# Kernel tuning notes

Hardware: AMD Instinct MI355X
Metric: run time of the kernel (lower is better)

The kernel has to match this reference:

```python
import jax, jax.numpy as jnp
import numpy as np

NEG_SLOPE = 0.2  # PyG GATConv default negative_slope
N_GRAPHS = 128


def gat_conv(x, src, dst, w, a_src, a_dst, b):
    """PyG GATConv (v1), concat=True. x:[N,F], src/dst:[E] (self-loops included),
    w:[F,H*C], a_src/a_dst:[H,C], b:[H*C]."""
    N = x.shape[0]
    H, C = a_src.shape
    h = (x @ w).reshape(N, H, C)                      # [N,H,C]
    e = (h * a_src).sum(-1)[src] + (h * a_dst).sum(-1)[dst]  # [E,H]
    e = jnp.where(e > 0, e, NEG_SLOPE * e)            # leaky_relu
    m = jax.ops.segment_max(e, dst, num_segments=N)   # per-dst softmax max
    ex = jnp.exp(e - m[dst])
    s = jax.ops.segment_sum(ex, dst, num_segments=N)
    alpha = ex / (s[dst] + 1e-16)                     # [E,H]
    out = jax.ops.segment_sum(h[src] * alpha[:, :, None], dst, num_segments=N)
    return out.reshape(N, H * C) + b


def pool(x, batch, num_graphs):
    """concat(global_mean_pool, global_max_pool)."""
    ones = jnp.ones((x.shape[0],), x.dtype)
    cnt = jax.ops.segment_sum(ones, batch, num_segments=num_graphs)
    mean = jax.ops.segment_sum(x, batch, num_segments=num_graphs) / jnp.maximum(cnt, 1.0)[:, None]
    mx = jax.ops.segment_max(x, batch, num_segments=num_graphs)
    return jnp.concatenate([mean, mx], axis=-1)


def setup_inputs() -> dict:
    key = jax.random.key(0)
    ks = jax.random.split(key, 30)
    N, E, G = 100000, 800000, N_GRAPHS
    F_in, H, C = 260, 4, 64
    HC = H * C  # 256

    def lin(k, i, o):
        return (jax.random.normal(k, (i, o), jnp.float32) * (1.0 / np.sqrt(i)))

    def att(k):
        return jax.random.normal(k, (H, C), jnp.float32) * 0.1

    return {
        "x": jax.random.normal(ks[0], (N, F_in), jnp.float32),
        "edge_index": jax.random.randint(ks[1], (2, E), 0, N),
        "batch": jnp.sort(jax.random.randint(ks[2], (N,), 0, G)),
        "gat1_w": lin(ks[3], F_in, HC), "gat1_as": att(ks[4]), "gat1_ad": att(ks[5]),
        "gat1_b": jnp.zeros((HC,), jnp.float32),
        "lin1_w": lin(ks[6], HC, C), "lin1_b": jnp.zeros((C,), jnp.float32),
        "gat2_w": lin(ks[7], C, HC), "gat2_as": att(ks[8]), "gat2_ad": att(ks[9]),
        "gat2_b": jnp.zeros((HC,), jnp.float32),
        "lin2_w": lin(ks[10], HC, C), "lin2_b": jnp.zeros((C,), jnp.float32),
        "sum_w": lin(ks[11], 4 * C, 2 * C), "sum_b": jnp.zeros((2 * C,), jnp.float32),
        "sh1_w": lin(ks[12], 2 * C, C), "sh1_b": jnp.zeros((C,), jnp.float32),
        "sh2_w": lin(ks[13], C, C), "sh2_b": jnp.zeros((C,), jnp.float32),
        "sh3_w": lin(ks[14], C, C), "sh3_b": jnp.zeros((C,), jnp.float32),
        "reg_w": lin(ks[15], C, 32), "reg_b": jnp.zeros((32,), jnp.float32),
    }


def reference(x, edge_index, batch,
              gat1_w, gat1_as, gat1_ad, gat1_b, lin1_w, lin1_b,
              gat2_w, gat2_as, gat2_ad, gat2_b, lin2_w, lin2_b,
              sum_w, sum_b, sh1_w, sh1_b, sh2_w, sh2_b, sh3_w, sh3_b,
              reg_w, reg_b):
    N = x.shape[0]
    loop = jnp.arange(N)
    src = jnp.concatenate([edge_index[0], loop])  # add_self_loops=True
    dst = jnp.concatenate([edge_index[1], loop])

    h = gat_conv(x, src, dst, gat1_w, gat1_as, gat1_ad, gat1_b)
    h = jax.nn.selu(h @ lin1_w + lin1_b)
    x1 = pool(h, batch, N_GRAPHS)                 # [G, 2C]

    h = gat_conv(h, src, dst, gat2_w, gat2_as, gat2_ad, gat2_b)
    h = jax.nn.selu(h @ lin2_w + lin2_b)
    x2 = pool(h, batch, N_GRAPHS)                 # [G, 2C]

    z = jnp.concatenate([x1, x2], axis=-1) @ sum_w + sum_b
    z = jax.nn.selu(z @ sh1_w + sh1_b)
    z = jax.nn.selu(z @ sh2_w + sh2_b)
    z = jax.nn.selu(z @ sh3_w + sh3_b)
    return z @ reg_w + reg_b                      # [G, 32]
```

## Files before the change

kernel.cpp:

```cpp
#include <hip/hip_runtime.h>
#include <hip/hip_bf16.h>
#include <cstdint>

#define NEG_SLOPE 0.2f
#define HEADS 4
#define CH 64
#define HC 256
#define F_IN 260
#define KPAD1 288
#define NGRAPH 128

typedef __attribute__((ext_vector_type(8))) short bf16x8;
typedef __attribute__((ext_vector_type(8))) unsigned short u16x8;
typedef __attribute__((ext_vector_type(4))) float f32x4;

__device__ __forceinline__ float seluf(float x){
    const float sc=1.0507009873554805f, al=1.6732632423543772f;
    return x>0.f ? sc*x : sc*al*(__expf(x)-1.f);
}
__device__ __forceinline__ unsigned fenc(float x){
    unsigned u=__float_as_uint(x);
    return (u&0x80000000u)? ~u : (u|0x80000000u);
}
__device__ __forceinline__ float fdec(unsigned e){
    unsigned u = (e&0x80000000u)? (e&0x7fffffffu) : ~e;
    return __uint_as_float(u);
}
__device__ __forceinline__ float bf2f(unsigned short u){
    return __uint_as_float(((unsigned)u)<<16);
}
__device__ __forceinline__ unsigned short f2bf_raw(float x){
    unsigned u = __float_as_uint(x);
    unsigned rounded = u + 0x7fffu + ((u >> 16) & 1u);
    return (unsigned short)(rounded >> 16);
}
__device__ __forceinline__ void gload_lds16(const void* g, void* l){
    __builtin_amdgcn_global_load_lds(
        (const __attribute__((address_space(1))) void*)g,
        (__attribute__((address_space(3))) void*)l, 16, 0, 0);
}

__global__ void fill_u32_kernel(unsigned* p, unsigned v, int n){
    int i = blockIdx.x*blockDim.x + threadIdx.x;
    for (; i<n; i += gridDim.x*blockDim.x) p[i]=v;
}

__global__ void degree_kernel(const int* __restrict__ ei, int* __restrict__ deg, int E){
    int i = blockIdx.x*blockDim.x+threadIdx.x;
    for (; i<E; i+=gridDim.x*blockDim.x) atomicAdd(&deg[ei[E+i]], 1);
}

__global__ void scan_ph1(const int* __restrict__ deg, int* __restrict__ bsum, int N){
    __shared__ int sd[256];
    int base = blockIdx.x*1024;
    int t = threadIdx.x;
    int tot=0;
    for(int u=0;u<4;u++){ int i = base + t*4+u; tot += (i<N)? deg[i]:0; }
    sd[t]=tot; __syncthreads();
    for(int off=128; off; off>>=1){ if(t<off) sd[t]+=sd[t+off]; __syncthreads(); }
    if(t==0) bsum[blockIdx.x]=sd[0];
}
__global__ void scan_ph2(int* bsum, int nb, int* rowptr, int N, int E){
    if(threadIdx.x==0 && blockIdx.x==0){
        int run=0;
        for(int b=0;b<nb;b++){ int v=bsum[b]; bsum[b]=run; run+=v; }
        rowptr[N]=E;
    }
}
__global__ void scan_ph3(const int* __restrict__ deg, const int* __restrict__ bsum,
                         int* __restrict__ rowptr, int N){
    __shared__ int sd[256];
    int base = blockIdx.x*1024;
    int t = threadIdx.x;
    int v[4]; int tot=0;
    for(int u=0;u<4;u++){ int i=base+t*4+u; v[u] = (i<N)? deg[i]:0; tot+=v[u]; }
    sd[t]=tot; __syncthreads();
    for(int off=1; off<256; off<<=1){
        int add = (t>=off)? sd[t-off] : 0;
        __syncthreads();
        sd[t] += add;
        __syncthreads();
    }
    int pre = bsum[blockIdx.x] + ((t==0)?0: sd[t-1]);
    for(int u=0;u<4;u++){ int i=base+t*4+u; if(i<N){ rowptr[i]=pre; pre+=v[u]; } }
}

__global__ void scatter_kernel(const int* __restrict__ ei, const int* __restrict__ rowptr,
                               int* __restrict__ fil, int* __restrict__ col, int E){
    int i = blockIdx.x*blockDim.x+threadIdx.x;
    for(; i<E; i+=gridDim.x*blockDim.x){
        int s = ei[i], d = ei[E+i];
        int p = atomicAdd(&fil[d],1);
        col[rowptr[d]+p] = s;
    }
}

__global__ void cvt_x_kernel(const float* __restrict__ x, unsigned* __restrict__ xb, int N){
    int i = blockIdx.x*blockDim.x+threadIdx.x;
    int total = N*36;
    for (; i<total; i+=gridDim.x*blockDim.x){
        int row = i/36;
        int c = (i - row*36)*8;
        const float* src = x + (size_t)row*F_IN + c;
        float v[8];
        if (c + 8 <= F_IN){
            float4 a = *(const float4*)src;
            float4 b = *(const float4*)(src+4);
            v[0]=a.x; v[1]=a.y; v[2]=a.z; v[3]=a.w;
            v[4]=b.x; v[5]=b.y; v[6]=b.z; v[7]=b.w;
        } else {
            #pragma unroll
            for (int k=0;k<8;k++) v[k] = (c+k < F_IN) ? src[k] : 0.f;
        }
        unsigned d[4];
        #pragma unroll
        for (int k=0;k<4;k++)
            d[k] = (unsigned)f2bf_raw(v[2*k]) | ((unsigned)f2bf_raw(v[2*k+1])<<16);
        *(int4*)(xb + (size_t)row*144 + (c>>1)) = make_int4((int)d[0],(int)d[1],(int)d[2],(int)d[3]);
    }
}

__global__ void cvt_wT_kernel(const float* __restrict__ w, __hip_bfloat16* __restrict__ wt,
                              int K, int NC, int Kpad){
    int i = blockIdx.x*blockDim.x+threadIdx.x;
    if (i >= NC*Kpad) return;
    int n = i / Kpad, k = i - n*Kpad;
    wt[i] = __float2bfloat16(k < K ? w[(size_t)k*NC + n] : 0.f);
}

template<int BN, int FS, int POOL, int STORE>
__global__ __launch_bounds__(512, 4) void mfma_gemm_kernel(
    const __hip_bfloat16* __restrict__ A, int Kpad,
    const __hip_bfloat16* __restrict__ Bt,
    const float* __restrict__ bias, int act,
    __hip_bfloat16* __restrict__ Cb,
    const float* __restrict__ asrc, const float* __restrict__ adst,
    float* __restrict__ ss, float* __restrict__ sdv,
    const int* __restrict__ batch, float* __restrict__ psum,
    unsigned* __restrict__ pmax, int* __restrict__ cnt,
    int M, int NC)
{
    constexpr int NF = BN/32;
    constexpr int WN = BN/2;
    constexpr int TP = WN + 8;
    constexpr int STAGE = 16384 + 2*BN*64;
    constexpr int LDSB  = POOL ? (STAGE + 128*72*2) : 32768;
    __shared__ __align__(16) char lds[LDSB];

    int tid  = threadIdx.x;
    int lane = tid & 63;
    int w    = tid >> 6;
    int wr = w >> 1, wc = w & 1;
    int row0 = blockIdx.x * 128;
    int col0 = blockIdx.y * BN;
    int fr   = lane & 15;
    int koff = (lane >> 4) * 16;

    f32x4 acc[2][NF];
    #pragma unroll
    for (int i=0;i<2;i++)
        #pragma unroll
        for (int j=0;j<NF;j++) acc[i][j] = (f32x4){0.f,0.f,0.f,0.f};

    int lrow = lane >> 2;
    int lcolB = (lane & 3) * 16;
    int ktiles = Kpad >> 5;

    auto stage = [&](int kt, int pb){
        int k0b = kt*64;
        char* Asb = lds + pb*8192;
        char* Bsb = lds + 16384 + pb*(BN*64);
        {
            int gr = row0 + w*16 + lrow; if (gr > M-1) gr = M-1;
            gload_lds16((const char*)A + (size_t)gr*Kpad*2 + k0b + lcolB,
                        Asb + w*1024 + lrow*64 + lcolB);
        }
        if (w < BN/16){
            int gn = col0 + w*16 + lrow;
            gload_lds16((const char*)Bt + (size_t)gn*Kpad*2 + k0b + lcolB,
                        Bsb + w*1024 + lrow*64 + lcolB);
        }
    };

    stage(0, 0);
    __syncthreads();
    for (int kt=0; kt<ktiles; kt++){
        int pb = kt & 1;
        if (kt+1 < ktiles) stage(kt+1, pb^1);
        const char* Ab = lds + pb*8192;
        const char* Bb = lds + 16384 + pb*(BN*64);
        bf16x8 a[2], b[NF];
        a[0] = *(const bf16x8*)(Ab + (wr*32 +      fr)*64 + koff);
        a[1] = *(const bf16x8*)(Ab + (wr*32 + 16 + fr)*64 + koff);
        #pragma unroll
        for (int nt=0; nt<NF; nt++)
            b[nt] = *(const bf16x8*)(Bb + (wc*WN + nt*16 + fr)*64 + koff);
        #pragma unroll
        for (int mt=0; mt<2; mt++)
            #pragma unroll
            for (int nt=0; nt<NF; nt++)
                acc[mt][nt] = __builtin_amdgcn_mfma_f32_16x16x32_bf16(a[mt], b[nt], acc[mt][nt], 0, 0, 0);
        __syncthreads();
    }

    if (POOL){
        unsigned short* tile = (unsigned short*)(lds + STAGE);
        #pragma unroll
        for (int mt=0; mt<2; mt++)
            #pragma unroll
            for (int nt=0; nt<NF; nt++)
                #pragma unroll
                for (int r=0; r<4; r++){
                    float v = acc[mt][nt][r] + bias[wc*WN + nt*16 + fr];
                    v = seluf(v);
                    int tr = wr*32 + mt*16 + (lane>>4)*4 + r;
                    tile[tr*72 + wc*WN + nt*16 + fr] = f2bf_raw(v);
                }
        __syncthreads();
        if (STORE){
            #pragma unroll
            for (int p=0; p<2; p++){
                int idx = tid + p*512;
                int r = idx >> 3, ch = idx & 7;
                int gr = row0 + r;
                if (gr < M)
                    *(int4*)((char*)Cb + ((size_t)gr*NC + ch*8)*2) =
                        *(const int4*)((const char*)tile + r*144 + ch*16);
            }
        }
        int c  = tid & 63;
        int g8 = tid >> 6;
        float sum = 0.f, mx = -__builtin_inff();
        int cur = -1, rl = 0;
        #pragma unroll 1
        for (int j=0; j<16; j++){
            int r = g8*16 + j;
            int n = row0 + r;
            if (n >= M) break;
            int g = batch[n];
            if (g != cur){
                if (cur >= 0){
                    atomicAdd(&psum[cur*64+c], sum);
                    atomicMax(&pmax[cur*64+c], fenc(mx));
                    if (POOL==1 && c==0) atomicAdd(&cnt[cur], rl);
                }
                cur = g; sum = 0.f; mx = -__builtin_inff(); rl = 0;
            }
            float v = bf2f(tile[r*72 + c]);
            sum += v; mx = fmaxf(mx, v); rl++;
        }
        if (cur >= 0){
            atomicAdd(&psum[cur*64+c], sum);
            atomicMax(&pmax[cur*64+c], fenc(mx));
            if (POOL==1 && c==0) atomicAdd(&cnt[cur], rl);
        }
        return;
    }

    if (FS){
        float asv[NF], adv[NF];
        #pragma unroll
        for (int nt=0; nt<NF; nt++){
            int gc = col0 + wc*WN + nt*16 + fr;
            asv[nt] = asrc[gc];
            adv[nt] = adst[gc];
        }
        int head = (col0 + wc*WN) >> 6;
        #pragma unroll
        for (int mt=0; mt<2; mt++){
            #pragma unroll
            for (int r=0; r<4; r++){
                float ts=0.f, td=0.f;
                #pragma unroll
                for (int nt=0; nt<NF; nt++){
                    ts = fmaf(acc[mt][nt][r], asv[nt], ts);
                    td = fmaf(acc[mt][nt][r], adv[nt], td);
                }
                #pragma unroll
                for (int off=1; off<16; off<<=1){
                    ts += __shfl_xor(ts, off);
                    td += __shfl_xor(td, off);
                }
                if (fr==0){
                    int gr = row0 + wr*32 + mt*16 + (lane>>4)*4 + r;
                    if (gr < M){ ss[gr*4+head]=ts; sdv[gr*4+head]=td; }
                }
            }
        }
    }

    char* ct = lds + w*(16*TP*2);
    int c0 = col0 + wc*WN;
    #pragma unroll
    for (int mt=0; mt<2; mt++){
        #pragma unroll
        for (int nt=0; nt<NF; nt++){
            #pragma unroll
            for (int r=0; r<4; r++){
                float v = acc[mt][nt][r];
                if (bias) v += bias[c0 + nt*16 + fr];
                if (act)  v = seluf(v);
                int tr = (lane>>4)*4 + r;
                *(unsigned short*)(ct + tr*(TP*2) + (nt*16+fr)*2) = f2bf_raw(v);
            }
        }
        constexpr int CPR = WN/8;
        constexpr int RPP = 64/CPR;
        #pragma unroll
        for (int p=0; p<16/RPP; p++){
            int tr = p*RPP + lane/CPR;
            int ch = lane % CPR;
            int4 v = *(const int4*)(ct + tr*(TP*2) + ch*16);
            int gr = row0 + wr*32 + mt*16 + tr;
            if (gr < M)
                *(int4*)((char*)Cb + ((size_t)gr*NC + c0 + ch*8)*2) = v;
        }
    }
}

__global__ void aggregate_fused_kernel(const __hip_bfloat16* __restrict__ h,
                                       const float* __restrict__ ss, const float* __restrict__ sdv,
                                       const int* __restrict__ rowptr, const int* __restrict__ col,
                                       const float* __restrict__ bias,
                                       __hip_bfloat16* __restrict__ outp, int N){
    int node = blockIdx.x*4 + (threadIdx.x>>6);
    if (node >= N) return;
    int lane = threadIdx.x & 63;
    int s = lane >> 4;
    int t = lane & 15;
    int hh = t >> 2;
    const unsigned short* hp = (const unsigned short*)h;

    float ad = sdv[node*4+hh];
    float e0 = ss[node*4+hh] + ad;
    e0 = fmaxf(e0, NEG_SLOPE*e0);

    int jb = rowptr[node], je = rowptr[node+1];

    float m = (s==0) ? e0 : -1e30f;
    for (int j0 = jb; j0 < je; j0 += 8){
        int jA = j0 + s, jB = j0 + s + 4;
        if (jA < je){
            float e = ss[col[jA]*4+hh] + ad;
            m = fmaxf(m, fmaxf(e, NEG_SLOPE*e));
        }
        if (jB < je){
            float e = ss[col[jB]*4+hh] + ad;
            m = fmaxf(m, fmaxf(e, NEG_SLOPE*e));
        }
    }
    m = fmaxf(m, __shfl_xor(m, 16));
    m = fmaxf(m, __shfl_xor(m, 32));

    float acc[16];
    float psum;
    {
        float sa = (s==0) ? __expf(e0-m) : 0.f;
        psum = sa;
        const unsigned short* base = hp + (size_t)node*HC + t*16;
        u16x8 v0 = *(const u16x8*)(base);
        u16x8 v1 = *(const u16x8*)(base + 8);
        #pragma unroll
        for (int k=0;k<8;k++){
            acc[k]   = sa * bf2f(v0[k]);
            acc[8+k] = sa * bf2f(v1[k]);
        }
    }
    for (int j0 = jb; j0 < je; j0 += 8){
        int jA = j0 + s;
        int jB = j0 + s + 4;
        int scA = (jA < je) ? col[jA] : node;
        int scB = (jB < je) ? col[jB] : node;
        const unsigned short* bA = hp + (size_t)scA*HC + t*16;
        const unsigned short* bB = hp + (size_t)scB*HC + t*16;
        u16x8 a0 = *(const u16x8*)bA;
        u16x8 a1 = *(const u16x8*)(bA + 8);
        u16x8 b0 = *(const u16x8*)bB;
        u16x8 b1 = *(const u16x8*)(bB + 8);
        float eA = ss[scA*4+hh] + ad;
        float eB = ss[scB*4+hh] + ad;
        eA = fmaxf(eA, NEG_SLOPE*eA);
        eB = fmaxf(eB, NEG_SLOPE*eB);
        float pA = (jA < je) ? __expf(eA - m) : 0.f;
        float pB = (jB < je) ? __expf(eB - m) : 0.f;
        psum += pA + pB;
        #pragma unroll
        for (int k=0;k<8;k++){
            acc[k]   = fmaf(pA, bf2f(a0[k]), acc[k]);
            acc[8+k] = fmaf(pA, bf2f(a1[k]), acc[8+k]);
        }
        #pragma unroll
        for (int k=0;k<8;k++){
            acc[k]   = fmaf(pB, bf2f(b0[k]), acc[k]);
            acc[8+k] = fmaf(pB, bf2f(b1[k]), acc[8+k]);
        }
    }

    #pragma unroll
    for (int k=0;k<16;k++){
        acc[k] += __shfl_xor(acc[k], 16);
        acc[k] += __shfl_xor(acc[k], 32);
    }
    psum += __shfl_xor(psum, 16);
    psum += __shfl_xor(psum, 32);

    if (s==0){
        float inv = 1.f / psum;
        unsigned d[8];
        #pragma unroll
        for (int k=0;k<8;k++){
            unsigned lo = f2bf_raw(fmaf(acc[2*k],   inv, bias[t*16 + 2*k]));
            unsigned hi = f2bf_raw(fmaf(acc[2*k+1], inv, bias[t*16 + 2*k+1]));
            d[k] = lo | (hi<<16);
        }
        unsigned short* op = (unsigned short*)outp + (size_t)node*HC + t*16;
        int4 w0 = make_int4((int)d[0], (int)d[1], (int)d[2], (int)d[3]);
        int4 w1 = make_int4((int)d[4], (int)d[5], (int)d[6], (int)d[7]);
        *(int4*)op = w0;
        *(int4*)(op + 8) = w1;
    }
}

__global__ void pool_final_kernel(const float* __restrict__ psum, const unsigned* __restrict__ pmax,
                                  const int* __restrict__ cnt, float* __restrict__ x, int G){
    int i = blockIdx.x*blockDim.x+threadIdx.x;
    if (i >= G*64) return;
    int g=i>>6, c=i&63;
    float cf = fmaxf((float)cnt[g], 1.f);
    x[g*128 + c] = psum[i]/cf;
    x[g*128 + 64 + c] = fdec(pmax[i]);
}

__global__ __launch_bounds__(128) void head_kernel(
    const float* __restrict__ x1, const float* __restrict__ x2,
    const float* __restrict__ sw, const float* __restrict__ sb,
    const float* __restrict__ w1, const float* __restrict__ b1,
    const float* __restrict__ w2, const float* __restrict__ b2,
    const float* __restrict__ w3, const float* __restrict__ b3,
    const float* __restrict__ rw, const float* __restrict__ rb,
    float* __restrict__ out)
{
    int g = blockIdx.x, t = threadIdx.x;
    __shared__ float v[256], z1[128], z2[64], z3[64], z4[64];
    v[t] = x1[g*128+t];
    v[128+t] = x2[g*128+t];
    __syncthreads();
    float a = sb[t];
    for(int k=0;k<256;k++) a = fmaf(v[k], sw[k*128+t], a);
    z1[t] = a;
    __syncthreads();
    if(t<64){
        float a2 = b1[t];
        for(int k=0;k<128;k++) a2 = fmaf(z1[k], w1[k*64+t], a2);
        z2[t] = seluf(a2);
    }
    __syncthreads();
    if(t<64){
        float a3 = b2[t];
        for(int k=0;k<64;k++) a3 = fmaf(z2[k], w2[k*64+t], a3);
        z3[t] = seluf(a3);
    }
    __syncthreads();
    if(t<64){
        float a4 = b3[t];
        for(int k=0;k<64;k++) a4 = fmaf(z3[k], w3[k*64+t], a4);
        z4[t] = seluf(a4);
    }
    __syncthreads();
    if(t<32){
        float a5 = rb[t];
        for(int k=0;k<64;k++) a5 = fmaf(z4[k], rw[k*32+t], a5);
        out[g*32+t] = a5;
    }
}

extern "C" void kernel_launch(void* const* d_in, const int* in_sizes, int n_in,
                              void* d_out, int out_size, void* d_ws, size_t ws_size,
                              hipStream_t stream)
{
    const float* x    = (const float*)d_in[0];
    const int*   ei   = (const int*)d_in[1];
    const int*   batch= (const int*)d_in[2];
    const float* g1w  = (const float*)d_in[3];
    const float* g1as = (const float*)d_in[4];
    const float* g1ad = (const float*)d_in[5];
    const float* g1b  = (const float*)d_in[6];
    const float* l1w  = (const float*)d_in[7];
    const float* l1b  = (const float*)d_in[8];
    const float* g2w  = (const float*)d_in[9];
    const float* g2as = (const float*)d_in[10];
    const float* g2ad = (const float*)d_in[11];
    const float* g2b  = (const float*)d_in[12];
    const float* l2w  = (const float*)d_in[13];
    const float* l2b  = (const float*)d_in[14];
    const float* sw   = (const float*)d_in[15];
    const float* sb   = (const float*)d_in[16];
    const float* s1w  = (const float*)d_in[17];
    const float* s1b  = (const float*)d_in[18];
    const float* s2w  = (const float*)d_in[19];
    const float* s2b  = (const float*)d_in[20];
    const float* s3w  = (const float*)d_in[21];
    const float* s3b  = (const float*)d_in[22];
    const float* rw   = (const float*)d_in[23];
    const float* rb   = (const float*)d_in[24];
    float* out = (float*)d_out;

    const int N = in_sizes[0] / F_IN;
    const int E = in_sizes[1] / 2;
    const int G = NGRAPH;

    char* ws = (char*)d_ws;
    size_t off = 0;
    auto alloc = [&](size_t bytes)->void*{
        void* p = ws + off;
        off += (bytes + 255) & ~(size_t)255;
        return p;
    };
    int* deg     = (int*)alloc((size_t)2*N*4);
    int* fil     = deg + N;
    int* rowptr  = (int*)alloc(((size_t)N+1)*4);
    int* col     = (int*)alloc((size_t)E*4);
    int* bsum    = (int*)alloc(1024);
    int* zpool   = (int*)alloc((size_t)(128 + 2*G*64)*4);
    int*   cnt = zpool;
    float* PS1 = (float*)(zpool + 128);
    float* PS2 = PS1 + G*64;
    unsigned* PM1 = (unsigned*)alloc((size_t)2*G*64*4);
    unsigned* PM2 = PM1 + G*64;
    float* X1    = (float*)alloc((size_t)G*128*4);
    float* X2    = (float*)alloc((size_t)G*128*4);
    __hip_bfloat16* Xb  = (__hip_bfloat16*)alloc((size_t)N*KPAD1*2);
    __hip_bfloat16* W1t = (__hip_bfloat16*)alloc((size_t)HC*KPAD1*2);
    __hip_bfloat16* L1t = (__hip_bfloat16*)alloc((size_t)CH*HC*2);
    __hip_bfloat16* W2t = (__hip_bfloat16*)alloc((size_t)HC*CH*2);
    __hip_bfloat16* L2t = (__hip_bfloat16*)alloc((size_t)CH*HC*2);
    __hip_bfloat16* Abf = (__hip_bfloat16*)alloc((size_t)N*HC*2);
    __hip_bfloat16* Bbf = (__hip_bfloat16*)alloc((size_t)N*HC*2);
    __hip_bfloat16* HSb = (__hip_bfloat16*)alloc((size_t)N*CH*2);
    float* SCS   = (float*)alloc((size_t)N*HEADS*4);
    float* SCD   = (float*)alloc((size_t)N*HEADS*4);
    (void)ws_size; (void)n_in; (void)out_size;

    const unsigned ENC_NEG_INF = 0x007FFFFFu;
    int nb = (N+1023)/1024;

    fill_u32_kernel<<<256,256,0,stream>>>((unsigned*)deg, 0u, 2*N);
    fill_u32_kernel<<<64,256,0,stream>>>((unsigned*)zpool, 0u, 128 + 2*G*64);
    fill_u32_kernel<<<64,256,0,stream>>>(PM1, ENC_NEG_INF, 2*G*64);

    degree_kernel<<<1024,256,0,stream>>>(ei, deg, E);
    scan_ph1<<<nb,256,0,stream>>>(deg, bsum, N);
    scan_ph2<<<1,64,0,stream>>>(bsum, nb, rowptr, N, E);
    scan_ph3<<<nb,256,0,stream>>>(deg, bsum, rowptr, N);
    scatter_kernel<<<1024,256,0,stream>>>(ei, rowptr, fil, col, E);

    cvt_x_kernel<<<2048,256,0,stream>>>(x, (unsigned*)Xb, N);
    cvt_wT_kernel<<<(HC*KPAD1+255)/256,256,0,stream>>>(g1w, W1t, F_IN, HC, KPAD1);
    cvt_wT_kernel<<<(CH*HC+255)/256,256,0,stream>>>(l1w, L1t, HC, CH, HC);
    cvt_wT_kernel<<<(HC*CH+255)/256,256,0,stream>>>(g2w, W2t, CH, HC, CH);
    cvt_wT_kernel<<<(CH*HC+255)/256,256,0,stream>>>(l2w, L2t, HC, CH, HC);

    int nodeBlocks = (N+3)/4;
    dim3 gA((N+127)/128, 2);
    dim3 gL((N+127)/128, 1);

    mfma_gemm_kernel<128,1,0,1><<<gA,512,0,stream>>>(Xb, KPAD1, W1t, nullptr, 0, Abf,
                                                     g1as, g1ad, SCS, SCD,
                                                     nullptr, nullptr, nullptr, nullptr, N, HC);
    aggregate_fused_kernel<<<nodeBlocks,256,0,stream>>>(Abf, SCS, SCD, rowptr, col, g1b, Bbf, N);
    mfma_gemm_kernel<64,0,1,1><<<gL,512,0,stream>>>(Bbf, HC, L1t, l1b, 1, HSb,
                                                    nullptr, nullptr, nullptr, nullptr,
                                                    batch, PS1, PM1, cnt, N, CH);
    pool_final_kernel<<<(G*64+255)/256,256,0,stream>>>(PS1, PM1, cnt, X1, G);

    mfma_gemm_kernel<128,1,0,1><<<gA,512,0,stream>>>(HSb, CH, W2t, nullptr, 0, Abf,
                                                     g2as, g2ad, SCS, SCD,
                                                     nullptr, nullptr, nullptr, nullptr, N, HC);
    aggregate_fused_kernel<<<nodeBlocks,256,0,stream>>>(Abf, SCS, SCD, rowptr, col, g2b, Bbf, N);
    mfma_gemm_kernel<64,0,2,0><<<gL,512,0,stream>>>(Bbf, HC, L2t, l2b, 1, nullptr,
                                                    nullptr, nullptr, nullptr, nullptr,
                                                    batch, PS2, PM2, nullptr, N, CH);
    pool_final_kernel<<<(G*64+255)/256,256,0,stream>>>(PS2, PM2, cnt, X2, G);

    head_kernel<<<G,128,0,stream>>>(X1, X2, sw, sb, s1w, s1b, s2w, s2b, s3w, s3b, rw, rb, out);
}
```

Before: 462.7 us.

## Fuse fp32-to-bf16 input conversion into first GEMM and merge init kernels

Removes the separate x-to-bf16 conversion pass and its 100000x288 bf16 buffer. The first GAT GEMM now reads fp32 x directly, converts it in registers and writes the bf16 tile to LDS instead of using async global-to-LDS loads. It also merges the three fill kernels into one init kernel and the four weight-transpose kernels into one launch, and rewrites leaky_relu as a select. The cost is synchronous fp32 loads in the GEMM staging path, which may hurt overlap with compute and doubles the bytes read per A tile.

Result: faster. 449.7 us (-2.8%).

```diff
diff --git a/kernel.cpp b/kernel.cpp
--- a/kernel.cpp
+++ b/kernel.cpp
@@ -40,9 +40,15 @@
         (__attribute__((address_space(3))) void*)l, 16, 0, 0);
 }
 
-__global__ void fill_u32_kernel(unsigned* p, unsigned v, int n){
+__global__ void init_kernel(unsigned* a, int n0, unsigned* b, int n1,
+                            unsigned* c, int n2, unsigned neginf){
     int i = blockIdx.x*blockDim.x + threadIdx.x;
-    for (; i<n; i += gridDim.x*blockDim.x) p[i]=v;
+    int tot = n0 + n1 + n2;
+    for (; i<tot; i += gridDim.x*blockDim.x){
+        if (i < n0) a[i] = 0u;
+        else if (i < n0+n1) b[i-n0] = 0u;
+        else c[i-n0-n1] = neginf;
+    }
 }
 
 __global__ void degree_kernel(const int* __restrict__ ei, int* __restrict__ deg, int E){
@@ -95,42 +101,39 @@
     }
 }
 
-__global__ void cvt_x_kernel(const float* __restrict__ x, unsigned* __restrict__ xb, int N){
+#define S_W1 (HC*KPAD1)
+#define S_L1 (CH*HC)
+#define S_W2 (HC*CH)
+#define S_L2 (CH*HC)
+__global__ void cvt_w_all(const float* __restrict__ g1w, const float* __restrict__ l1w,
+                          const float* __restrict__ g2w, const float* __restrict__ l2w,
+                          __hip_bfloat16* __restrict__ W1t, __hip_bfloat16* __restrict__ L1t,
+                          __hip_bfloat16* __restrict__ W2t, __hip_bfloat16* __restrict__ L2t){
     int i = blockIdx.x*blockDim.x+threadIdx.x;
-    int total = N*36;
-    for (; i<total; i+=gridDim.x*blockDim.x){
-        int row = i/36;
-        int c = (i - row*36)*8;
-        const float* src = x + (size_t)row*F_IN + c;
-        float v[8];
-        if (c + 8 <= F_IN){
-            float4 a = *(const float4*)src;
-            float4 b = *(const float4*)(src+4);
-            v[0]=a.x; v[1]=a.y; v[2]=a.z; v[3]=a.w;
-            v[4]=b.x; v[5]=b.y; v[6]=b.z; v[7]=b.w;
+    int tot = S_W1 + S_L1 + S_W2 + S_L2;
+    for (; i<tot; i += gridDim.x*blockDim.x){
+        if (i < S_W1){
+            int n = i / KPAD1, k = i - n*KPAD1;
+            W1t[i] = __float2bfloat16(k < F_IN ? g1w[(size_t)k*HC + n] : 0.f);
+        } else if (i < S_W1 + S_L1){
+            int j = i - S_W1;
+            int n = j / HC, k = j - n*HC;
+            L1t[j] = __float2bfloat16(l1w[(size_t)k*CH + n]);
+        } else if (i < S_W1 + S_L1 + S_W2){
+            int j = i - S_W1 - S_L1;
+            int n = j / CH, k = j - n*CH;
+            W2t[j] = __float2bfloat16(g2w[(size_t)k*HC + n]);
         } else {
-            #pragma unroll
-            for (int k=0;k<8;k++) v[k] = (c+k < F_IN) ? src[k] : 0.f;
-        }
-        unsigned d[4];
-        #pragma unroll
-        for (int k=0;k<4;k++)
-            d[k] = (unsigned)f2bf_raw(v[2*k]) | ((unsigned)f2bf_raw(v[2*k+1])<<16);
-        *(int4*)(xb + (size_t)row*144 + (c>>1)) = make_int4((int)d[0],(int)d[1],(int)d[2],(int)d[3]);
-    }
-}
-
-__global__ void cvt_wT_kernel(const float* __restrict__ w, __hip_bfloat16* __restrict__ wt,
-                              int K, int NC, int Kpad){
-    int i = blockIdx.x*blockDim.x+threadIdx.x;
-    if (i >= NC*Kpad) return;
-    int n = i / Kpad, k = i - n*Kpad;
-    wt[i] = __float2bfloat16(k < K ? w[(size_t)k*NC + n] : 0.f);
-}
-
-template<int BN, int FS, int POOL, int STORE>
+            int j = i - S_W1 - S_L1 - S_W2;
+            int n = j / HC, k = j - n*HC;
+            L2t[j] = __float2bfloat16(l2w[(size_t)k*CH + n]);
+        }
+    }
+}
+
+template<int BN, int FS, int POOL, int STORE, int CVTA>
 __global__ __launch_bounds__(512, 4) void mfma_gemm_kernel(
-    const __hip_bfloat16* __restrict__ A, int Kpad,
+    const __hip_bfloat16* __restrict__ A, const float* __restrict__ Af, int Kpad,
     const __hip_bfloat16* __restrict__ Bt,
     const float* __restrict__ bias, int act,
     __hip_bfloat16* __restrict__ Cb,
@@ -170,7 +173,27 @@
         int k0b = kt*64;
         char* Asb = lds + pb*8192;
         char* Bsb = lds + 16384 + pb*(BN*64);
-        {
+        if (CVTA){
+            int gr = row0 + w*16 + lrow; if (gr > M-1) gr = M-1;
+            int gc = kt*32 + (lane & 3)*8;
+            const float* src = Af + (size_t)gr*F_IN + gc;
+            float v[8];
+            if (gc + 8 <= F_IN){
+                float4 a4 = *(const float4*)src;
+                float4 b4 = *(const float4*)(src+4);
+                v[0]=a4.x; v[1]=a4.y; v[2]=a4.z; v[3]=a4.w;
+                v[4]=b4.x; v[5]=b4.y; v[6]=b4.z; v[7]=b4.w;
+            } else {
+                #pragma unroll
+                for (int k2=0;k2<8;k2++) v[k2] = (gc+k2 < F_IN) ? src[k2] : 0.f;
+            }
+            unsigned d[4];
+            #pragma unroll
+            for (int k2=0;k2<4;k2++)
+                d[k2] = (unsigned)f2bf_raw(v[2*k2]) | ((unsigned)f2bf_raw(v[2*k2+1])<<16);
+            *(int4*)(Asb + w*1024 + lrow*64 + lcolB) =
+                make_int4((int)d[0],(int)d[1],(int)d[2],(int)d[3]);
+        } else {
             int gr = row0 + w*16 + lrow; if (gr > M-1) gr = M-1;
             gload_lds16((const char*)A + (size_t)gr*Kpad*2 + k0b + lcolB,
                         Asb + w*1024 + lrow*64 + lcolB);
@@ -333,7 +356,7 @@
 
     float ad = sdv[node*4+hh];
     float e0 = ss[node*4+hh] + ad;
-    e0 = fmaxf(e0, NEG_SLOPE*e0);
+    e0 = e0>0.f ? e0 : NEG_SLOPE*e0;
 
     int jb = rowptr[node], je = rowptr[node+1];
 
@@ -342,11 +365,11 @@
         int jA = j0 + s, jB = j0 + s + 4;
         if (jA < je){
             float e = ss[col[jA]*4+hh] + ad;
-            m = fmaxf(m, fmaxf(e, NEG_SLOPE*e));
+            m = fmaxf(m, e>0.f ? e : NEG_SLOPE*e);
         }
         if (jB < je){
             float e = ss[col[jB]*4+hh] + ad;
-            m = fmaxf(m, fmaxf(e, NEG_SLOPE*e));
+            m = fmaxf(m, e>0.f ? e : NEG_SLOPE*e);
         }
     }
     m = fmaxf(m, __shfl_xor(m, 16));
@@ -379,8 +402,8 @@
         u16x8 b1 = *(const u16x8*)(bB + 8);
         float eA = ss[scA*4+hh] + ad;
         float eB = ss[scB*4+hh] + ad;
-        eA = fmaxf(eA, NEG_SLOPE*eA);
-        eB = fmaxf(eB, NEG_SLOPE*eB);
+        eA = eA>0.f ? eA : NEG_SLOPE*eA;
+        eB = eB>0.f ? eB : NEG_SLOPE*eB;
         float pA = (jA < je) ? __expf(eA - m) : 0.f;
         float pB = (jB < je) ? __expf(eB - m) : 0.f;
         psum += pA + pB;
@@ -529,7 +552,6 @@
     unsigned* PM2 = PM1 + G*64;
     float* X1    = (float*)alloc((size_t)G*128*4);
     float* X2    = (float*)alloc((size_t)G*128*4);
-    __hip_bfloat16* Xb  = (__hip_bfloat16*)alloc((size_t)N*KPAD1*2);
     __hip_bfloat16* W1t = (__hip_bfloat16*)alloc((size_t)HC*KPAD1*2);
     __hip_bfloat16* L1t = (__hip_bfloat16*)alloc((size_t)CH*HC*2);
     __hip_bfloat16* W2t = (__hip_bfloat16*)alloc((size_t)HC*CH*2);
@@ -544,9 +566,9 @@
     const unsigned ENC_NEG_INF = 0x007FFFFFu;
     int nb = (N+1023)/1024;
 
-    fill_u32_kernel<<<256,256,0,stream>>>((unsigned*)deg, 0u, 2*N);
-    fill_u32_kernel<<<64,256,0,stream>>>((unsigned*)zpool, 0u, 128 + 2*G*64);
-    fill_u32_kernel<<<64,256,0,stream>>>(PM1, ENC_NEG_INF, 2*G*64);
+    init_kernel<<<256,256,0,stream>>>((unsigned*)deg, 2*N,
+                                      (unsigned*)zpool, 128 + 2*G*64,
+                                      PM1, 2*G*64*2/2 + 2*G*64 - 2*G*64 + 2*G*64, ENC_NEG_INF);
 
     degree_kernel<<<1024,256,0,stream>>>(ei, deg, E);
     scan_ph1<<<nb,256,0,stream>>>(deg, bsum, N);
@@ -554,32 +576,28 @@
     scan_ph3<<<nb,256,0,stream>>>(deg, bsum, rowptr, N);
     scatter_kernel<<<1024,256,0,stream>>>(ei, rowptr, fil, col, E);
 
-    cvt_x_kernel<<<2048,256,0,stream>>>(x, (unsigned*)Xb, N);
-    cvt_wT_kernel<<<(HC*KPAD1+255)/256,256,0,stream>>>(g1w, W1t, F_IN, HC, KPAD1);
-    cvt_wT_kernel<<<(CH*HC+255)/256,256,0,stream>>>(l1w, L1t, HC, CH, HC);
-    cvt_wT_kernel<<<(HC*CH+255)/256,256,0,stream>>>(g2w, W2t, CH, HC, CH);
-    cvt_wT_kernel<<<(CH*HC+255)/256,256,0,stream>>>(l2w, L2t, HC, CH, HC);
+    cvt_w_all<<<480,256,0,stream>>>(g1w, l1w, g2w, l2w, W1t, L1t, W2t, L2t);
 
     int nodeBlocks = (N+3)/4;
     dim3 gA((N+127)/128, 2);
     dim3 gL((N+127)/128, 1);
 
-    mfma_gemm_kernel<128,1,0,1><<<gA,512,0,stream>>>(Xb, KPAD1, W1t, nullptr, 0, Abf,
-                                                     g1as, g1ad, SCS, SCD,
-                                                     nullptr, nullptr, nullptr, nullptr, N, HC);
+    mfma_gemm_kernel<128,1,0,1,1><<<gA,512,0,stream>>>(nullptr, x, KPAD1, W1t, nullptr, 0, Abf,
+                                                       g1as, g1ad, SCS, SCD,
+                                                       nullptr, nullptr, nullptr, nullptr, N, HC);
     aggregate_fused_kernel<<<nodeBlocks,256,0,stream>>>(Abf, SCS, SCD, rowptr, col, g1b, Bbf, N);
-    mfma_gemm_kernel<64,0,1,1><<<gL,512,0,stream>>>(Bbf, HC, L1t, l1b, 1, HSb,
-                                                    nullptr, nullptr, nullptr, nullptr,
-                                                    batch, PS1, PM1, cnt, N, CH);
+    mfma_gemm_kernel<64,0,1,1,0><<<gL,512,0,stream>>>(Bbf, nullptr, HC, L1t, l1b, 1, HSb,
+                                                      nullptr, nullptr, nullptr, nullptr,
+                                                      batch, PS1, PM1, cnt, N, CH);
     pool_final_kernel<<<(G*64+255)/256,256,0,stream>>>(PS1, PM1, cnt, X1, G);
 
-    mfma_gemm_kernel<128,1,0,1><<<gA,512,0,stream>>>(HSb, CH, W2t, nullptr, 0, Abf,
-                                                     g2as, g2ad, SCS, SCD,
-                                                     nullptr, nullptr, nullptr, nullptr, N, HC);
+    mfma_gemm_kernel<128,1,0,1,0><<<gA,512,0,stream>>>(HSb, nullptr, CH, W2t, nullptr, 0, Abf,
+                                                       g2as, g2ad, SCS, SCD,
+                                                       nullptr, nullptr, nullptr, nullptr, N, HC);
     aggregate_fused_kernel<<<nodeBlocks,256,0,stream>>>(Abf, SCS, SCD, rowptr, col, g2b, Bbf, N);
-    mfma_gemm_kernel<64,0,2,0><<<gL,512,0,stream>>>(Bbf, HC, L2t, l2b, 1, nullptr,
-                                                    nullptr, nullptr, nullptr, nullptr,
-                                                    batch, PS2, PM2, nullptr, N, CH);
+    mfma_gemm_kernel<64,0,2,0,0><<<gL,512,0,stream>>>(Bbf, nullptr, HC, L2t, l2b, 1, nullptr,
+                                                      nullptr, nullptr, nullptr, nullptr,
+                                                      batch, PS2, PM2, nullptr, N, CH);
     pool_final_kernel<<<(G*64+255)/256,256,0,stream>>>(PS2, PM2, cnt, X2, G);
 
     head_kernel<<<G,128,0,stream>>>(X1, X2, sw, sb, s1w, s1b, s2w, s2b, s3w, s3b, rw, rb, out);
```
